# Optimization experiments

Measured on AMD Instinct MI355X. Metric: run time of the kernel, lower is better.

Reference implementation:

```python
import jax, jax.numpy as jnp
import numpy as np

B = 2; S, H, W = 14, 28, 28; C = 128; NH = 8; WS = 7; SH = 3
N = WS ** 3            # 343 tokens per window
HID = 4 * C            # 512 MLP hidden
EPS = 1e-5
SCALE = (C // NH) ** -0.5


def _rel_index():
    # reproduces the torch code exactly (meshgrid indexing='xy', quirky strides)
    coords = np.stack(np.meshgrid(np.arange(WS), np.arange(WS), np.arange(WS), indexing='xy'))  # (3,7,7,7)
    flat = coords.reshape(3, -1)                              # (3, N)
    rel = flat[:, :, None] - flat[:, None, :]                 # (3, N, N)
    rel = rel.transpose(1, 2, 0).astype(np.int64)             # (N, N, 3)
    rel[..., 0] += WS - 1
    rel[..., 1] += WS - 1
    rel[..., 2] += WS - 1
    rel[..., 0] *= 3 * WS - 1
    rel[..., 1] *= 2 * WS - 1
    return rel.sum(-1)                                        # (N, N)


def _attn_mask():
    # standard shifted-window mask: 0 where same region, -100 otherwise
    img = np.zeros((S, H, W), np.float32)
    sl = (slice(0, -WS), slice(-WS, -SH), slice(-SH, None))
    cnt = 0
    for a in sl:
        for b in sl:
            for c in sl:
                img[a, b, c] = cnt
                cnt += 1
    mw = img.reshape(S // WS, WS, H // WS, WS, W // WS, WS)
    mw = mw.transpose(0, 2, 4, 1, 3, 5).reshape(-1, N)        # (nW, N)
    am = mw[:, None, :] - mw[:, :, None]
    return jnp.asarray(np.where(am != 0, -100.0, 0.0).astype(np.float32))


def setup_inputs() -> dict:
    key = jax.random.key(0)
    ks = jax.random.split(key, 8)
    rn = lambda k, shp, s=0.02: jax.random.normal(k, shp, jnp.float32) * s
    return {
        'x': jax.random.normal(ks[0], (B, S * H * W, C), jnp.float32),
        'mask_matrix': _attn_mask(),
        'g1': jnp.ones((C,), jnp.float32), 'b1': jnp.zeros((C,), jnp.float32),
        'qkv_w': rn(ks[1], (C, 3 * C)), 'qkv_b': jnp.zeros((3 * C,), jnp.float32),
        'rpb': rn(ks[2], ((2 * WS - 1) ** 3, NH)),
        'proj_w': rn(ks[3], (C, C)), 'proj_b': jnp.zeros((C,), jnp.float32),
        'g2': jnp.ones((C,), jnp.float32), 'b2': jnp.zeros((C,), jnp.float32),
        'fc1_w': rn(ks[4], (C, HID)), 'fc1_b': jnp.zeros((HID,), jnp.float32),
        'fc2_w': rn(ks[5], (HID, C)), 'fc2_b': jnp.zeros((C,), jnp.float32),
        'rel_index': jnp.asarray(_rel_index(), jnp.int32),
    }


def _ln(x, g, b):
    mu = x.mean(-1, keepdims=True)
    d = x - mu
    var = (d * d).mean(-1, keepdims=True)
    return d * jax.lax.rsqrt(var + EPS) * g + b


def reference(x, mask_matrix, g1, b1, qkv_w, qkv_b, rpb, proj_w, proj_b,
              g2, b2, fc1_w, fc1_b, fc2_w, fc2_b, rel_index):
    shortcut = x
    h = _ln(x, g1, b1).reshape(B, S, H, W, C)
    h = jnp.roll(h, (-SH, -SH, -SH), axis=(1, 2, 3))
    # window partition -> (B_, N, C)
    h = h.reshape(B, S // WS, WS, H // WS, WS, W // WS, WS, C)
    h = h.transpose(0, 1, 3, 5, 2, 4, 6, 7).reshape(-1, N, C)
    B_ = h.shape[0]
    qkv = (h @ qkv_w + qkv_b).reshape(B_, N, 3, NH, C // NH).transpose(2, 0, 3, 1, 4)
    q, k, v = qkv[0] * SCALE, qkv[1], qkv[2]
    attn = jnp.einsum('bhnd,bhmd->bhnm', q, k)                # (B_, NH, N, N)
    bias = rpb[rel_index.reshape(-1)].reshape(N, N, NH).transpose(2, 0, 1)
    attn = attn + bias[None]
    nW = mask_matrix.shape[0]
    attn = attn.reshape(B_ // nW, nW, NH, N, N) + mask_matrix[None, :, None]
    attn = jax.nn.softmax(attn.reshape(B_, NH, N, N), axis=-1)
    o = jnp.einsum('bhnm,bhmd->bnhd', attn, v).reshape(B_, N, C)
    o = o @ proj_w + proj_b
    # window reverse -> (B, S, H, W, C)
    o = o.reshape(B, S // WS, H // WS, W // WS, WS, WS, WS, C)
    o = o.transpose(0, 1, 4, 2, 5, 3, 6, 7).reshape(B, S, H, W, C)
    o = jnp.roll(o, (SH, SH, SH), axis=(1, 2, 3)).reshape(B, S * H * W, C)
    x = shortcut + o
    y = _ln(x, g2, b2)
    y = jax.nn.gelu(y @ fc1_w + fc1_b, approximate=False) @ fc2_w + fc2_b
    return x + y
```

## Files before the change

### kernel.cpp

```cpp
#include <hip/hip_runtime.h>
#include <hip/hip_bf16.h>
#include <math.h>

typedef _Float16 half2_t __attribute__((ext_vector_type(2)));
typedef _Float16 half4_t __attribute__((ext_vector_type(4)));
typedef _Float16 half8_t __attribute__((ext_vector_type(8)));
typedef float float4_t __attribute__((ext_vector_type(4)));

#define MFMA16(a,b,c) __builtin_amdgcn_mfma_f32_16x16x16f16((a),(b),(c),0,0,0)
#define MFMA32(a,b,c) __builtin_amdgcn_mfma_f32_16x16x32_f16((a),(b),(c),0,0,0)

static __device__ __forceinline__ half2_t cvt_pk(float a, float b) {
  return __builtin_bit_cast(half2_t, __builtin_amdgcn_cvt_pkrtz(a, b));
}

static constexpr int NTOK = 21952;
static constexpr int NREG = 5488;
static constexpr float LOG2E = 1.44269504088896340736f;

__device__ __forceinline__ int rid_of(int cls, int n) {
  int z = n / 49, r = n - z*49, y = r / 7, x = r - y*7;
  int rs = (cls & 4) ? (z < 4 ? 1 : 2) : 0;
  int rh = (cls & 2) ? (y < 4 ? 1 : 2) : 0;
  int rw = (cls & 1) ? (x < 4 ? 1 : 2) : 0;
  return rs*9 + rh*3 + rw;
}

__global__ __launch_bounds__(256) void k_precomp(
    const float* __restrict__ qkv_w, const float* __restrict__ proj_w,
    const float* __restrict__ fc1_w, const float* __restrict__ fc2_w,
    const float* __restrict__ rpb,
    _Float16* __restrict__ qkv_wT, _Float16* __restrict__ proj_wT,
    _Float16* __restrict__ fc1_wT, _Float16* __restrict__ fc2_wT,
    _Float16* __restrict__ biasT, unsigned* __restrict__ bmask)
{
  int i = blockIdx.x * 256 + threadIdx.x;
  if (i < 49152) { int n = i >> 7, k = i & 127; qkv_wT[i] = (_Float16)qkv_w[k*384 + n]; return; }
  i -= 49152;
  if (i < 16384) { int n = i >> 7, k = i & 127; proj_wT[i] = (_Float16)proj_w[k*128 + n]; return; }
  i -= 16384;
  if (i < 65536) { int n = i >> 7, k = i & 127; fc1_wT[i] = (_Float16)fc1_w[k*512 + n]; return; }
  i -= 65536;
  if (i < 65536) { int n = i >> 9, k = i & 511; fc2_wT[i] = (_Float16)fc2_w[k*128 + n]; return; }
  i -= 65536;
  if (i < 8*343*352) {
    int h = i / (343*352); int r = i - h*343*352; int q = r / 352; int k = r - q*352;
    _Float16 v;
    if (k >= 343) v = (_Float16)(-30000.f);
    else {
      int zq = q/49, rq_ = q - zq*49, yq = rq_/7, xq = rq_ - yq*7;
      int zk = k/49, rk_ = k - zk*49, yk = rk_/7, xk = rk_ - yk*7;
      int idx = 20*(yq - yk + 6) + 13*(zq - zk + 6) + (xq - xk + 6);
      v = (_Float16)(rpb[idx*8 + h] * LOG2E);
    }
    biasT[i] = v;
    return;
  }
  i -= 8*343*352;
  if (i < 8*343*11) {
    int cls = i / (343*11); int r = i - cls*343*11; int q = r / 11; int kt = r - q*11;
    int rq = rid_of(cls, q);
    unsigned wbits = 0u;
    for (int j = 0; j < 32; ++j) {
      int k = kt*32 + j;
      if (k < 343 && rid_of(cls, k) == rq) wbits |= (1u << j);
    }
    bmask[i] = wbits;
  }
}

__device__ __forceinline__ void qkv_store(int row, int col, float v,
    const float* __restrict__ bias, _Float16* __restrict__ outh)
{
  v += bias[col];
  int which = col >> 7;
  if (which == 0) v *= 0.25f;
  int hh = (col >> 4) & 7, d = col & 15;
  int w = row / 343, n = row - w*343;
  size_t base = (size_t)((which*64 + w)*8 + hh)*NREG;
  if (which == 2) outh[base + d*343 + n] = (_Float16)v;
  else            outh[base + n*16  + d] = (_Float16)v;
}

__global__ __launch_bounds__(384) void k_qkv(
    const float* __restrict__ x, const float* __restrict__ g1, const float* __restrict__ b1,
    const _Float16* __restrict__ qkv_wT, const float* __restrict__ qkv_b,
    _Float16* __restrict__ qkvb)
{
  __shared__ _Float16 A[32][136];
  int mt = blockIdx.x;
  int tid = threadIdx.x, wid = tid >> 6, lane = tid & 63;
  for (int r = wid; r < 32; r += 6) {
    int row = mt*32 + r;
    int w = row / 343, n = row - w*343;
    int b = w >> 5, widx = w & 31;
    int sz = widx >> 4, sy = (widx >> 2) & 3, sx = widx & 3;
    int z = n / 49, rem = n - z*49, y = rem / 7, xx = rem - y*7;
    int gs = sz*7 + z + 3;  if (gs >= 14) gs -= 14;
    int gh = sy*7 + y + 3;  if (gh >= 28) gh -= 28;
    int gw = sx*7 + xx + 3; if (gw >= 28) gw -= 28;
    int gt = b*10976 + (gs*28 + gh)*28 + gw;
    const float* xr = x + (size_t)gt*128;
    float2 v = *(const float2*)(xr + lane*2);
    float s = v.x + v.y, sq = v.x*v.x + v.y*v.y;
    #pragma unroll
    for (int o = 1; o < 64; o <<= 1) { s += __shfl_xor(s, o); sq += __shfl_xor(sq, o); }
    float mu = s * 0.0078125f;
    float rstd = rsqrtf(sq*0.0078125f - mu*mu + 1e-5f);
    int c = lane*2;
    half2_t hv = { (_Float16)((v.x-mu)*rstd*g1[c]   + b1[c]),
                   (_Float16)((v.y-mu)*rstd*g1[c+1] + b1[c+1]) };
    *(half2_t*)&A[r][c] = hv;
  }
  __syncthreads();
  int lo = lane & 15, grp = lane >> 4;
  const _Float16* bp = qkv_wT + (size_t)(wid*64 + lo)*128 + grp*8;
  float4_t a00={0,0,0,0}, a01={0,0,0,0}, a02={0,0,0,0}, a03={0,0,0,0};
  float4_t a10={0,0,0,0}, a11={0,0,0,0}, a12={0,0,0,0}, a13={0,0,0,0};
  #pragma unroll
  for (int kk = 0; kk < 128; kk += 32) {
    half8_t f0 = *(const half8_t*)&A[lo][kk + grp*8];
    half8_t f1 = *(const half8_t*)&A[16 + lo][kk + grp*8];
    half8_t b0 = *(const half8_t*)(bp + kk);
    half8_t b1 = *(const half8_t*)(bp + kk + (size_t)16*128);
    half8_t b2 = *(const half8_t*)(bp + kk + (size_t)32*128);
    half8_t b3 = *(const half8_t*)(bp + kk + (size_t)48*128);
    a00 = MFMA32(f0, b0, a00);  a01 = MFMA32(f0, b1, a01);
    a02 = MFMA32(f0, b2, a02);  a03 = MFMA32(f0, b3, a03);
    a10 = MFMA32(f1, b0, a10);  a11 = MFMA32(f1, b1, a11);
    a12 = MFMA32(f1, b2, a12);  a13 = MFMA32(f1, b3, a13);
  }
  int row0 = mt*32 + grp*4;
  int colb = wid*64 + lo;
  #pragma unroll
  for (int r = 0; r < 4; ++r) {
    qkv_store(row0+r,    colb,    a00[r], qkv_b, qkvb);
    qkv_store(row0+r,    colb+16, a01[r], qkv_b, qkvb);
    qkv_store(row0+r,    colb+32, a02[r], qkv_b, qkvb);
    qkv_store(row0+r,    colb+48, a03[r], qkv_b, qkvb);
    qkv_store(row0+16+r, colb,    a10[r], qkv_b, qkvb);
    qkv_store(row0+16+r, colb+16, a11[r], qkv_b, qkvb);
    qkv_store(row0+16+r, colb+32, a12[r], qkv_b, qkvb);
    qkv_store(row0+16+r, colb+48, a13[r], qkv_b, qkvb);
  }
}

__global__ __launch_bounds__(512) void k_attn(
    const _Float16* __restrict__ qkv, const _Float16* __restrict__ biasT,
    const unsigned* __restrict__ bmask, _Float16* __restrict__ obuf)
{
  __shared__ _Float16 Klds[352][24];
  __shared__ _Float16 VTlds[16][360];
  int bx = blockIdx.x;
  int w = bx >> 3, h = bx & 7;
  int b = w >> 5, widx = w & 31;
  int sz = widx >> 4, sy = (widx >> 2) & 3, sx = widx & 3;
  int cls = (sz << 2) | (sy == 3 ? 2 : 0) | (sx == 3 ? 1 : 0);
  int tid = threadIdx.x;
  const _Float16* qp  = qkv + (size_t)(w*8 + h) * NREG;
  const _Float16* kp  = qp + (size_t)512  * NREG;
  const _Float16* vtp = qp + (size_t)1024 * NREG;
  for (int c = tid; c < 704; c += 512) {
    int n = c >> 1, d0 = (c & 1) * 8;
    half8_t kv = {};
    if (n < 343) kv = *(const half8_t*)(kp + n*16 + d0);
    *(half8_t*)&Klds[n][d0] = kv;
  }
  for (int c = tid; c < 704; c += 512) {
    int d = c / 44, n0 = (c - d*44) * 8;
    half8_t vv = {};
    if (n0 + 8 <= 343) vv = *(const half8_t*)(vtp + d*343 + n0);
    else { for (int j = 0; j < 8; ++j) vv[j] = (n0 + j < 343) ? vtp[d*343 + n0 + j] : (_Float16)0.f; }
    *(half8_t*)&VTlds[d][n0] = vv;
  }
  __syncthreads();
  int lane = tid & 63, lo = lane & 15, grp = lane >> 4;
  int wid = tid >> 6;
  for (int qt = wid; qt < 22; qt += 8) {
    int q  = qt*16 + lo;
    int qv = q < 343 ? q : 342;
    half4_t qf = *(const half4_t*)(qp + (size_t)qv*16 + grp*4);
    const _Float16* bp  = biasT + (size_t)(h*343 + qv)*352;
    const unsigned* bmp = bmask + (size_t)(cls*343 + qv)*11;
    half4_t barr0[11], barr1[11];
    unsigned bmarr[11];
    #pragma unroll
    for (int kt = 0; kt < 11; ++kt) {
      barr0[kt] = *(const half4_t*)(bp + kt*32 + grp*4);
      barr1[kt] = *(const half4_t*)(bp + kt*32 + 16 + grp*4);
      bmarr[kt] = bmp[kt];
    }
    float lsum = 0.f;
    float4_t acc = {0.f, 0.f, 0.f, 0.f};
    #pragma unroll
    for (int kt = 0; kt < 11; ++kt) {
      int kb = kt*32;
      half4_t ka0 = *(const half4_t*)&Klds[kb + lo][grp*4];
      half4_t ka1 = *(const half4_t*)&Klds[kb + 16 + lo][grp*4];
      float4_t zero = {0.f, 0.f, 0.f, 0.f};
      float4_t s0 = MFMA16(ka0, qf, zero);
      float4_t s1 = MFMA16(ka1, qf, zero);
      unsigned bmw = bmarr[kt];
      float p[8];
      #pragma unroll
      for (int i = 0; i < 8; ++i) {
        float sv = (i < 4) ? s0[i] : s1[i-4];
        float bb = (float)((i < 4) ? barr0[kt][i] : barr1[kt][i-4]);
        float e = exp2f(fmaf(sv, LOG2E, bb));
        unsigned bit = (bmw >> ((i >> 2)*16 + grp*4 + (i & 3))) & 1u;
        p[i] = bit ? e : 0.f;
        lsum += p[i];
      }
      half2_t pk01 = cvt_pk(p[0], p[1]);
      half2_t pk23 = cvt_pk(p[2], p[3]);
      half2_t pk45 = cvt_pk(p[4], p[5]);
      half2_t pk67 = cvt_pk(p[6], p[7]);
      half4_t pb0 = __builtin_shufflevector(pk01, pk23, 0, 1, 2, 3);
      half4_t pb1 = __builtin_shufflevector(pk45, pk67, 0, 1, 2, 3);
      half4_t va0 = *(const half4_t*)&VTlds[lo][kb + grp*4];
      half4_t va1 = *(const half4_t*)&VTlds[lo][kb + 16 + grp*4];
      acc = MFMA16(va0, pb0, acc);
      acc = MFMA16(va1, pb1, acc);
    }
    lsum += __shfl_xor(lsum, 16);
    lsum += __shfl_xor(lsum, 32);
    if (q < 343) {
      int z = q/49, rem = q - z*49, y = rem/7, xx = rem - y*7;
      int gs = sz*7 + z + 3;  if (gs >= 14) gs -= 14;
      int gh = sy*7 + y + 3;  if (gh >= 28) gh -= 28;
      int gw = sx*7 + xx + 3; if (gw >= 28) gw -= 28;
      int gt = b*10976 + (gs*28 + gh)*28 + gw;
      float rl = 1.f / lsum;
      half4_t o4 = { (_Float16)(acc[0]*rl), (_Float16)(acc[1]*rl),
                     (_Float16)(acc[2]*rl), (_Float16)(acc[3]*rl) };
      *(half4_t*)(obuf + (size_t)gt*128 + h*16 + grp*4) = o4;
    }
  }
}

__global__ __launch_bounds__(512) void k_mlp(
    const _Float16* __restrict__ obuf, const _Float16* __restrict__ proj_wT,
    const float* __restrict__ proj_b, const float* __restrict__ x,
    const float* __restrict__ g2, const float* __restrict__ b2,
    const _Float16* __restrict__ fc1_wT, const float* __restrict__ fc1_b,
    float* __restrict__ x2, _Float16* __restrict__ hid)
{
  __shared__ _Float16 P[32][136];
  __shared__ float    X2[32][132];
  int mt = blockIdx.x;
  int tid = threadIdx.x, wid = tid >> 6, lane = tid & 63, lo = lane & 15, grp = lane >> 4;
  for (int r = wid; r < 32; r += 8) {
    int row = mt*32 + r;
    half2_t v = *(const half2_t*)(obuf + (size_t)row*128 + lane*2);
    *(half2_t*)&P[r][lane*2] = v;
  }
  __syncthreads();
  {
    const _Float16* bp = proj_wT + (size_t)(wid*16 + lo)*128 + grp*8;
    float4_t a0={0,0,0,0}, a1={0,0,0,0};
    #pragma unroll
    for (int kk = 0; kk < 128; kk += 32) {
      half8_t f0 = *(const half8_t*)&P[lo][kk + grp*8];
      half8_t f1 = *(const half8_t*)&P[16 + lo][kk + grp*8];
      half8_t b0 = *(const half8_t*)(bp + kk);
      a0 = MFMA32(f0, b0, a0);
      a1 = MFMA32(f1, b0, a1);
    }
    int colb = wid*16 + lo;
    float bb = proj_b[colb];
    #pragma unroll
    for (int r = 0; r < 4; ++r) {
      int r0 = grp*4 + r;
      int row0 = mt*32 + r0, row1 = row0 + 16;
      float w0 = x[(size_t)row0*128 + colb] + a0[r] + bb;
      float w1 = x[(size_t)row1*128 + colb] + a1[r] + bb;
      x2[(size_t)row0*128 + colb] = w0;  X2[r0][colb]    = w0;
      x2[(size_t)row1*128 + colb] = w1;  X2[r0+16][colb] = w1;
    }
  }
  __syncthreads();
  for (int r = wid; r < 32; r += 8) {
    float2 v = { X2[r][lane*2], X2[r][lane*2 + 1] };
    float s = v.x + v.y, sq = v.x*v.x + v.y*v.y;
    #pragma unroll
    for (int o = 1; o < 64; o <<= 1) { s += __shfl_xor(s, o); sq += __shfl_xor(sq, o); }
    float mu = s * 0.0078125f;
    float rstd = rsqrtf(sq*0.0078125f - mu*mu + 1e-5f);
    int c = lane*2;
    half2_t hv = { (_Float16)((v.x-mu)*rstd*g2[c]   + b2[c]),
                   (_Float16)((v.y-mu)*rstd*g2[c+1] + b2[c+1]) };
    *(half2_t*)&P[r][c] = hv;
  }
  __syncthreads();
  {
    const _Float16* bp = fc1_wT + (size_t)(wid*64 + lo)*128 + grp*8;
    float4_t a00={0,0,0,0}, a01={0,0,0,0}, a02={0,0,0,0}, a03={0,0,0,0};
    float4_t a10={0,0,0,0}, a11={0,0,0,0}, a12={0,0,0,0}, a13={0,0,0,0};
    #pragma unroll
    for (int kk = 0; kk < 128; kk += 32) {
      half8_t f0 = *(const half8_t*)&P[lo][kk + grp*8];
      half8_t f1 = *(const half8_t*)&P[16 + lo][kk + grp*8];
      half8_t b0 = *(const half8_t*)(bp + kk);
      half8_t b1 = *(const half8_t*)(bp + kk + (size_t)16*128);
      half8_t b2 = *(const half8_t*)(bp + kk + (size_t)32*128);
      half8_t b3 = *(const half8_t*)(bp + kk + (size_t)48*128);
      a00 = MFMA32(f0, b0, a00);  a01 = MFMA32(f0, b1, a01);
      a02 = MFMA32(f0, b2, a02);  a03 = MFMA32(f0, b3, a03);
      a10 = MFMA32(f1, b0, a10);  a11 = MFMA32(f1, b1, a11);
      a12 = MFMA32(f1, b2, a12);  a13 = MFMA32(f1, b3, a13);
    }
    int row0 = mt*32 + grp*4;
    int colb = wid*64 + lo;
    #pragma unroll
    for (int r = 0; r < 4; ++r) {
      float vv[8] = { a00[r], a01[r], a02[r], a03[r], a10[r], a11[r], a12[r], a13[r] };
      #pragma unroll
      for (int j = 0; j < 8; ++j) {
        int rr  = row0 + r + (j >= 4 ? 16 : 0);
        int col = colb + (j & 3)*16;
        float v = vv[j] + fc1_b[col];
        float g = 0.5f * v * (1.0f + erff(v * 0.70710678118654752f));
        hid[(size_t)rr*512 + col] = (_Float16)g;
      }
    }
  }
}

__global__ __launch_bounds__(256) void k_fc2(
    const _Float16* __restrict__ hid, const _Float16* __restrict__ fc2_wT,
    const float* __restrict__ fc2_b, const float* __restrict__ x2,
    float* __restrict__ out)
{
  int gw = blockIdx.x*4 + (threadIdx.x >> 6);
  int nb = gw / 1372;
  int mt = gw - nb*1372;
  int lane = threadIdx.x & 63, lo = lane & 15, grp = lane >> 4;
  const _Float16* ap = hid + (size_t)(mt*16 + lo)*512 + grp*8;
  const _Float16* bp = fc2_wT + (size_t)(nb*64 + lo)*512 + grp*8;
  float4_t acc0 = {0,0,0,0}, acc1 = {0,0,0,0}, acc2 = {0,0,0,0}, acc3 = {0,0,0,0};
  for (int kk = 0; kk < 512; kk += 32) {
    half8_t a  = *(const half8_t*)(ap + kk);
    half8_t b0 = *(const half8_t*)(bp + kk);
    half8_t b1 = *(const half8_t*)(bp + kk + (size_t)16*512);
    half8_t b2 = *(const half8_t*)(bp + kk + (size_t)32*512);
    half8_t b3 = *(const half8_t*)(bp + kk + (size_t)48*512);
    acc0 = MFMA32(a, b0, acc0);
    acc1 = MFMA32(a, b1, acc1);
    acc2 = MFMA32(a, b2, acc2);
    acc3 = MFMA32(a, b3, acc3);
  }
  int rowb = mt*16 + grp*4;
  int colb = nb*64 + lo;
  #pragma unroll
  for (int r = 0; r < 4; ++r) {
    int row = rowb + r;
    out[(size_t)row*128 + colb]      = x2[(size_t)row*128 + colb]      + acc0[r] + fc2_b[colb];
    out[(size_t)row*128 + colb + 16] = x2[(size_t)row*128 + colb + 16] + acc1[r] + fc2_b[colb+16];
    out[(size_t)row*128 + colb + 32] = x2[(size_t)row*128 + colb + 32] + acc2[r] + fc2_b[colb+32];
    out[(size_t)row*128 + colb + 48] = x2[(size_t)row*128 + colb + 48] + acc3[r] + fc2_b[colb+48];
  }
}

extern "C" void kernel_launch(void* const* d_in, const int* in_sizes, int n_in,
                              void* d_out, int out_size, void* d_ws, size_t ws_size,
                              hipStream_t stream)
{
  const float* x      = (const float*)d_in[0];
  const float* g1     = (const float*)d_in[2];
  const float* b1     = (const float*)d_in[3];
  const float* qkv_w  = (const float*)d_in[4];
  const float* qkv_b  = (const float*)d_in[5];
  const float* rpb    = (const float*)d_in[6];
  const float* proj_w = (const float*)d_in[7];
  const float* proj_b = (const float*)d_in[8];
  const float* g2     = (const float*)d_in[9];
  const float* b2     = (const float*)d_in[10];
  const float* fc1_w  = (const float*)d_in[11];
  const float* fc1_b  = (const float*)d_in[12];
  const float* fc2_w  = (const float*)d_in[13];
  const float* fc2_b  = (const float*)d_in[14];
  char* ws = (char*)d_ws;
  size_t o = 0;
  auto alloc = [&](size_t bytes) { size_t r = o; o += (bytes + 255) & ~size_t(255); return r; };
  size_t oOB  = alloc((size_t)NTOK*128*2);
  size_t oX2  = alloc((size_t)NTOK*128*4);
  size_t oU   = alloc((size_t)NTOK*512*2);
  size_t oWQ  = alloc(49152*2);
  size_t oWP  = alloc(16384*2);
  size_t oW1  = alloc(65536*2);
  size_t oW2  = alloc(65536*2);
  size_t oBT  = alloc((size_t)8*343*352*2);
  size_t oBM  = alloc((size_t)8*343*11*4);
  (void)ws_size; (void)in_sizes; (void)n_in; (void)out_size;
  _Float16* obuf   = (_Float16*)(ws + oOB);
  float*    x2     = (float*)(ws + oX2);
  _Float16* qkvb   = (_Float16*)(ws + oU);
  _Float16* hid    = (_Float16*)(ws + oU);
  _Float16* qkv_wT = (_Float16*)(ws + oWQ);
  _Float16* proj_wT= (_Float16*)(ws + oWP);
  _Float16* fc1_wT = (_Float16*)(ws + oW1);
  _Float16* fc2_wT = (_Float16*)(ws + oW2);
  _Float16* biasT  = (_Float16*)(ws + oBT);
  unsigned* bmask  = (unsigned*)(ws + oBM);
  float*    out    = (float*)d_out;

  k_precomp<<<4662, 256, 0, stream>>>(qkv_w, proj_w, fc1_w, fc2_w, rpb,
                                      qkv_wT, proj_wT, fc1_wT, fc2_wT, biasT, bmask);
  k_qkv<<<686, 384, 0, stream>>>(x, g1, b1, qkv_wT, qkv_b, qkvb);
  k_attn<<<512, 512, 0, stream>>>(qkvb, biasT, bmask, obuf);
  k_mlp<<<686, 512, 0, stream>>>(obuf, proj_wT, proj_b, x, g2, b2,
                                 fc1_wT, fc1_b, x2, hid);
  k_fc2<<<686, 256, 0, stream>>>(hid, fc2_wT, fc2_b, x2, out);
}
```

Before: 126.9 us.

## Fuse fc2 GEMM into MLP kernel keeping hidden activations in shared memory

Merges the separate fc2 kernel into k_mlp. The GELU output is now written to a 32x520 fp16 shared tile, and the x2 residual stays in shared memory instead of making a round trip through global memory. This removes the global writes and reads of the hidden buffer (NTOK x 512 fp16) and of x2 (fp32), plus one kernel launch. In exchange, shared memory per block grows by about 33KB, which may lower occupancy. The fc2 GEMM also now runs with 8 waves per 32-row tile, each wave streaming a 16x512 weight slice.

```diff
diff --git a/kernel.cpp b/kernel.cpp
--- a/kernel.cpp
+++ b/kernel.cpp
@@ -243,10 +243,12 @@
     const float* __restrict__ proj_b, const float* __restrict__ x,
     const float* __restrict__ g2, const float* __restrict__ b2,
     const _Float16* __restrict__ fc1_wT, const float* __restrict__ fc1_b,
-    float* __restrict__ x2, _Float16* __restrict__ hid)
+    const _Float16* __restrict__ fc2_wT, const float* __restrict__ fc2_b,
+    float* __restrict__ out)
 {
   __shared__ _Float16 P[32][136];
   __shared__ float    X2[32][132];
+  __shared__ _Float16 H[32][520];
   int mt = blockIdx.x;
   int tid = threadIdx.x, wid = tid >> 6, lane = tid & 63, lo = lane & 15, grp = lane >> 4;
   for (int r = wid; r < 32; r += 8) {
@@ -272,10 +274,8 @@
     for (int r = 0; r < 4; ++r) {
       int r0 = grp*4 + r;
       int row0 = mt*32 + r0, row1 = row0 + 16;
-      float w0 = x[(size_t)row0*128 + colb] + a0[r] + bb;
-      float w1 = x[(size_t)row1*128 + colb] + a1[r] + bb;
-      x2[(size_t)row0*128 + colb] = w0;  X2[r0][colb]    = w0;
-      x2[(size_t)row1*128 + colb] = w1;  X2[r0+16][colb] = w1;
+      X2[r0][colb]    = x[(size_t)row0*128 + colb] + a0[r] + bb;
+      X2[r0+16][colb] = x[(size_t)row1*128 + colb] + a1[r] + bb;
     }
   }
   __syncthreads();
@@ -309,55 +309,41 @@
       a10 = MFMA32(f1, b0, a10);  a11 = MFMA32(f1, b1, a11);
       a12 = MFMA32(f1, b2, a12);  a13 = MFMA32(f1, b3, a13);
     }
-    int row0 = mt*32 + grp*4;
     int colb = wid*64 + lo;
     #pragma unroll
     for (int r = 0; r < 4; ++r) {
       float vv[8] = { a00[r], a01[r], a02[r], a03[r], a10[r], a11[r], a12[r], a13[r] };
       #pragma unroll
       for (int j = 0; j < 8; ++j) {
-        int rr  = row0 + r + (j >= 4 ? 16 : 0);
+        int rr  = grp*4 + r + (j >= 4 ? 16 : 0);
         int col = colb + (j & 3)*16;
         float v = vv[j] + fc1_b[col];
         float g = 0.5f * v * (1.0f + erff(v * 0.70710678118654752f));
-        hid[(size_t)rr*512 + col] = (_Float16)g;
+        H[rr][col] = (_Float16)g;
       }
     }
   }
-}
-
-__global__ __launch_bounds__(256) void k_fc2(
-    const _Float16* __restrict__ hid, const _Float16* __restrict__ fc2_wT,
-    const float* __restrict__ fc2_b, const float* __restrict__ x2,
-    float* __restrict__ out)
-{
-  int gw = blockIdx.x*4 + (threadIdx.x >> 6);
-  int nb = gw / 1372;
-  int mt = gw - nb*1372;
-  int lane = threadIdx.x & 63, lo = lane & 15, grp = lane >> 4;
-  const _Float16* ap = hid + (size_t)(mt*16 + lo)*512 + grp*8;
-  const _Float16* bp = fc2_wT + (size_t)(nb*64 + lo)*512 + grp*8;
-  float4_t acc0 = {0,0,0,0}, acc1 = {0,0,0,0}, acc2 = {0,0,0,0}, acc3 = {0,0,0,0};
-  for (int kk = 0; kk < 512; kk += 32) {
-    half8_t a  = *(const half8_t*)(ap + kk);
-    half8_t b0 = *(const half8_t*)(bp + kk);
-    half8_t b1 = *(const half8_t*)(bp + kk + (size_t)16*512);
-    half8_t b2 = *(const half8_t*)(bp + kk + (size_t)32*512);
-    half8_t b3 = *(const half8_t*)(bp + kk + (size_t)48*512);
-    acc0 = MFMA32(a, b0, acc0);
-    acc1 = MFMA32(a, b1, acc1);
-    acc2 = MFMA32(a, b2, acc2);
-    acc3 = MFMA32(a, b3, acc3);
-  }
-  int rowb = mt*16 + grp*4;
-  int colb = nb*64 + lo;
-  #pragma unroll
-  for (int r = 0; r < 4; ++r) {
-    int row = rowb + r;
-    out[(size_t)row*128 + colb]      = x2[(size_t)row*128 + colb]      + acc0[r] + fc2_b[colb];
-    out[(size_t)row*128 + colb + 16] = x2[(size_t)row*128 + colb + 16] + acc1[r] + fc2_b[colb+16];
-    out[(size_t)row*128 + colb + 32] = x2[(size_t)row*128 + colb + 32] + acc2[r] + fc2_b[colb+32];
-    out[(size_t)row*128 + colb + 48] = x2[(size_t)row*128 + colb + 48] + acc3[r] + fc2_b[colb+48];
+  __syncthreads();
+  {
+    const _Float16* bp = fc2_wT + (size_t)(wid*16 + lo)*512 + grp*8;
+    float4_t c0={0,0,0,0}, c1={0,0,0,0};
+    #pragma unroll
+    for (int kk = 0; kk < 512; kk += 32) {
+      half8_t f0 = *(const half8_t*)&H[lo][kk + grp*8];
+      half8_t f1 = *(const half8_t*)&H[16 + lo][kk + grp*8];
+      half8_t b0 = *(const half8_t*)(bp + kk);
+      c0 = MFMA32(f0, b0, c0);
+      c1 = MFMA32(f1, b0, c1);
+    }
+    int colb = wid*16 + lo;
+    float bb = fc2_b[colb];
+    #pragma unroll
+    for (int r = 0; r < 4; ++r) {
+      int r0 = grp*4 + r;
+      int row0 = mt*32 + r0;
+      out[(size_t)row0*128 + colb]      = X2[r0][colb]    + c0[r] + bb;
+      out[(size_t)(row0+16)*128 + colb] = X2[r0+16][colb] + c1[r] + bb;
+    }
   }
 }
 
@@ -383,7 +369,6 @@
   size_t o = 0;
   auto alloc = [&](size_t bytes) { size_t r = o; o += (bytes + 255) & ~size_t(255); return r; };
   size_t oOB  = alloc((size_t)NTOK*128*2);
-  size_t oX2  = alloc((size_t)NTOK*128*4);
   size_t oU   = alloc((size_t)NTOK*512*2);
   size_t oWQ  = alloc(49152*2);
   size_t oWP  = alloc(16384*2);
@@ -393,9 +378,7 @@
   size_t oBM  = alloc((size_t)8*343*11*4);
   (void)ws_size; (void)in_sizes; (void)n_in; (void)out_size;
   _Float16* obuf   = (_Float16*)(ws + oOB);
-  float*    x2     = (float*)(ws + oX2);
   _Float16* qkvb   = (_Float16*)(ws + oU);
-  _Float16* hid    = (_Float16*)(ws + oU);
   _Float16* qkv_wT = (_Float16*)(ws + oWQ);
   _Float16* proj_wT= (_Float16*)(ws + oWP);
   _Float16* fc1_wT = (_Float16*)(ws + oW1);
@@ -409,6 +392,5 @@
   k_qkv<<<686, 384, 0, stream>>>(x, g1, b1, qkv_wT, qkv_b, qkvb);
   k_attn<<<512, 512, 0, stream>>>(qkvb, biasT, bmask, obuf);
   k_mlp<<<686, 512, 0, stream>>>(obuf, proj_wT, proj_b, x, g2, b2,
-                                 fc1_wT, fc1_b, x2, hid);
-  k_fc2<<<686, 256, 0, stream>>>(hid, fc2_wT, fc2_b, x2, out);
-}
+                                 fc1_wT, fc1_b, fc2_wT, fc2_b, out);
+}
```

Result: faster. 106.3 us (-16.2%).
